# Optimization experiments

Hardware: AMD Instinct MI355X
Metric: run time of the kernel (lower is better)

The kernel has to match this reference:

```python
import jax, jax.numpy as jnp
import numpy as np

B, N, K, H = 512, 8192, 16, 16


def setup_inputs() -> dict:
    key = jax.random.key(0)
    ks = jax.random.split(key, 6)
    x = (2.0 * jax.random.bernoulli(ks[0], 0.5, (B, N)) - 1.0).astype(jnp.float32)
    neighs = jax.random.randint(ks[1], (N, K), 0, N, dtype=jnp.int32)  # per-site neighbor lists
    s1 = 1.0 / np.sqrt(K)
    s2 = 1.0 / np.sqrt(H)
    W1 = jax.random.uniform(ks[2], (N, K, H), jnp.float32, -s1, s1)
    b1 = jax.random.uniform(ks[3], (N, H), jnp.float32, -s1, s1)
    W2 = jax.random.uniform(ks[4], (N, H), jnp.float32, -s2, s2)
    b2 = jax.random.uniform(ks[5], (N,), jnp.float32, -s2, s2)
    return {"x": x, "neighs": neighs, "W1": W1, "b1": b1, "W2": W2, "b2": b2}


def reference(x, neighs, W1, b1, W2, b2):
    # Vectorized form of: for each site n, gather its K neighbors from x,
    # run a site-specific MLP [K -> H -> 1] (ReLU hidden, sigmoid output),
    # and scatter the scalar into x_hat[:, n].
    gathered = x[:, neighs]                                   # [B, N, K]
    h = jax.nn.relu(jnp.einsum('bnk,nkh->bnh', gathered, W1) + b1)  # [B, N, H]
    x_hat = jax.nn.sigmoid(jnp.einsum('bnh,nh->bn', h, W2) + b2)    # [B, N]
    return x_hat
```

## Files before the change

kernel.cpp:

```cpp
#include <hip/hip_runtime.h>
#include <stdint.h>

#define BB 512
#define NN 8192
#define KK 16
#define HH 16

typedef _Float16 f16;
typedef _Float16 f16x4 __attribute__((ext_vector_type(4)));
typedef float f32x4 __attribute__((ext_vector_type(4)));
typedef uint32_t u32x2 __attribute__((ext_vector_type(2)));

__global__ __launch_bounds__(256) void pack_kernel(const float* __restrict__ x,
                                                   uint32_t* __restrict__ xpT) {
    const int j = blockIdx.x * 256 + threadIdx.x;
    const int w = blockIdx.y;
    uint32_t word = 0u;
#pragma unroll
    for (int i = 0; i < 32; ++i)
        word |= (x[(size_t)(w * 32 + i) * NN + j] > 0.0f ? 1u : 0u) << i;
    xpT[(size_t)j * 16 + w] = word;
}

__global__ __launch_bounds__(256, 4) void mfma_kernel(
    const uint32_t* __restrict__ xpT, const int* __restrict__ neighs,
    const float* __restrict__ W1, const float* __restrict__ b1,
    const float* __restrict__ W2, const float* __restrict__ b2,
    float* __restrict__ out) {
    __shared__ int jtab[4][64];
    __shared__ __align__(16) uint32_t wbuf[4][4][32];
    __shared__ float tile[64][20];

    const int tid = threadIdx.x;
    const int wv  = __builtin_amdgcn_readfirstlane(tid >> 6);
    const int l   = tid & 63;
    const int l15 = l & 15;
    const int lg  = l >> 4;
    const int n0  = blockIdx.x * 16;
    const int b0  = blockIdx.y * 64;
    const int w0  = blockIdx.y * 2;

    jtab[wv][l] = neighs[(n0 + wv * 4) * KK + l];

#pragma unroll
    for (int ni = 0; ni < 4; ++ni) {
        const int n = n0 + wv * 4 + ni;

        if (l < 32) {
            const int j = jtab[wv][ni * 16 + (l & 15)];
            wbuf[wv][ni][l] = xpT[(size_t)j * 16 + w0 + (l >> 4)];
        }

        const float* W1n = W1 + (size_t)n * (KK * HH) + lg * 4 * HH + l15;
        f16x4 a;
#pragma unroll
        for (int i = 0; i < 4; ++i) a[i] = (f16)W1n[i * HH];

        const float4 b1v = *(const float4*)(b1 + (size_t)n * HH + lg * 4);
        const f32x4 cinit = {b1v.x, b1v.y, b1v.z, b1v.w};
        const float4 w2v = *(const float4*)(W2 + (size_t)n * HH + lg * 4);
        const float b2n = b2[n];

#pragma unroll
        for (int tb = 0; tb < 4; ++tb) {
            const uint4 wk =
                *(const uint4*)&wbuf[wv][ni][(tb >> 1) * 16 + lg * 4];
            const int pos = (tb & 1) * 16 + l15;
            const uint32_t d0 = 0xBC00BC00u ^ (((wk.x >> pos) & 1u) << 15) ^
                                (((wk.y >> pos) & 1u) << 31);
            const uint32_t d1 = 0xBC00BC00u ^ (((wk.z >> pos) & 1u) << 15) ^
                                (((wk.w >> pos) & 1u) << 31);
            const u32x2 bd = {d0, d1};
            const f16x4 bfr = __builtin_bit_cast(f16x4, bd);

            const f32x4 acc =
                __builtin_amdgcn_mfma_f32_16x16x16f16(a, bfr, cinit, 0, 0, 0);

            float z = fmaf(fmaxf(acc[0], 0.f), w2v.x,
                      fmaf(fmaxf(acc[1], 0.f), w2v.y,
                      fmaf(fmaxf(acc[2], 0.f), w2v.z,
                           fmaxf(acc[3], 0.f) * w2v.w)));
            z += __shfl_xor(z, 16);
            z += __shfl_xor(z, 32);
            z += b2n;
            const float r = 1.0f / (1.0f + __expf(-z));
            if (l < 16) tile[tb * 16 + l][wv * 4 + ni] = r;
        }
    }
    __syncthreads();

    const int row = tid >> 2;
    const int cg  = tid & 3;
    const float4 v = *(const float4*)&tile[row][cg * 4];
    *(float4*)(out + (size_t)(b0 + row) * NN + n0 + cg * 4) = v;
}

__global__ __launch_bounds__(512) void scalar_kernel(
    const float* __restrict__ x, const int* __restrict__ neighs,
    const float* __restrict__ W1, const float* __restrict__ b1,
    const float* __restrict__ W2, const float* __restrict__ b2,
    float* __restrict__ outp) {
    const int n = blockIdx.x;
    const int b = threadIdx.x;
    const int* nb = neighs + n * KK;
    const float* W1n = W1 + (size_t)n * KK * HH;
    const float* b1n = b1 + (size_t)n * HH;
    const float* W2n = W2 + (size_t)n * HH;

    float s[KK];
#pragma unroll
    for (int k = 0; k < KK; ++k) s[k] = x[(size_t)b * NN + nb[k]];

    float acc[HH];
#pragma unroll
    for (int h = 0; h < HH; ++h) acc[h] = b1n[h];
#pragma unroll
    for (int k = 0; k < KK; ++k)
#pragma unroll
        for (int h = 0; h < HH; ++h)
            acc[h] = fmaf(s[k], W1n[k * HH + h], acc[h]);

    float z = b2[n];
#pragma unroll
    for (int h = 0; h < HH; ++h)
        z = fmaf(fmaxf(acc[h], 0.0f), W2n[h], z);
    outp[(size_t)b * NN + n] = 1.0f / (1.0f + __expf(-z));
}

extern "C" void kernel_launch(void* const* d_in, const int* in_sizes, int n_in,
                              void* d_out, int out_size, void* d_ws, size_t ws_size,
                              hipStream_t stream) {
    const float* x      = (const float*)d_in[0];
    const int*   neighs = (const int*)d_in[1];
    const float* W1     = (const float*)d_in[2];
    const float* b1     = (const float*)d_in[3];
    const float* W2     = (const float*)d_in[4];
    const float* b2     = (const float*)d_in[5];
    float* out = (float*)d_out;

    const size_t pack_bytes = (size_t)NN * 16 * sizeof(uint32_t);

    if (ws_size >= pack_bytes) {
        uint32_t* xpT = (uint32_t*)d_ws;
        pack_kernel<<<dim3(NN / 256, BB / 32), 256, 0, stream>>>(x, xpT);
        mfma_kernel<<<dim3(NN / 16, BB / 64), 256, 0, stream>>>(
            xpT, neighs, W1, b1, W2, b2, out);
    } else {
        scalar_kernel<<<NN, BB, 0, stream>>>(x, neighs, W1, b1, W2, b2, out);
    }
}
```

Measured before the change: 31.13 us.

## Process the full batch per block so each site's weights load once

The MFMA kernel grid changes from (N/16, B/64) blocks of 256 threads to N/16 blocks of 512 threads, and each block now covers all 512 batch rows for 16 sites. Each wave handles 2 sites and runs 32 MFMA tiles per site instead of 4. It gathers all 16 packed batch words per neighbour into padded LDS, and the output tile covers 512 rows. This removes the re-reading of W1, b1, W2 and neighbour indices across the 8 batch blocks. In exchange there are fewer, larger blocks, about 40KB more LDS per block, and a long serial MFMA chain per wave.

Result: slower. 34.89 us (+12.1%).

```diff
diff --git a/kernel.cpp b/kernel.cpp
--- a/kernel.cpp
+++ b/kernel.cpp
@@ -22,14 +22,13 @@
     xpT[(size_t)j * 16 + w] = word;
 }
 
-__global__ __launch_bounds__(256, 4) void mfma_kernel(
+__global__ __launch_bounds__(512, 4) void mfma_kernel(
     const uint32_t* __restrict__ xpT, const int* __restrict__ neighs,
     const float* __restrict__ W1, const float* __restrict__ b1,
     const float* __restrict__ W2, const float* __restrict__ b2,
     float* __restrict__ out) {
-    __shared__ int jtab[4][64];
-    __shared__ __align__(16) uint32_t wbuf[4][4][32];
-    __shared__ float tile[64][20];
+    __shared__ __align__(16) uint32_t wbuf[8][2][16 * 20];
+    __shared__ __align__(16) float tile[512][20];
 
     const int tid = threadIdx.x;
     const int wv  = __builtin_amdgcn_readfirstlane(tid >> 6);
@@ -37,18 +36,17 @@
     const int l15 = l & 15;
     const int lg  = l >> 4;
     const int n0  = blockIdx.x * 16;
-    const int b0  = blockIdx.y * 64;
-    const int w0  = blockIdx.y * 2;
-
-    jtab[wv][l] = neighs[(n0 + wv * 4) * KK + l];
 
 #pragma unroll
-    for (int ni = 0; ni < 4; ++ni) {
-        const int n = n0 + wv * 4 + ni;
+    for (int ni = 0; ni < 2; ++ni) {
+        const int n = n0 + wv * 2 + ni;
+        uint32_t* wb = &wbuf[wv][ni][0];
 
-        if (l < 32) {
-            const int j = jtab[wv][ni * 16 + (l & 15)];
-            wbuf[wv][ni][l] = xpT[(size_t)j * 16 + w0 + (l >> 4)];
+#pragma unroll
+        for (int q = 0; q < 4; ++q) {
+            const int k = q * 4 + lg;
+            const int j = neighs[n * KK + k];
+            wb[l15 * 20 + k] = xpT[(size_t)j * 16 + l15];
         }
 
         const float* W1n = W1 + (size_t)n * (KK * HH) + lg * 4 * HH + l15;
@@ -62,10 +60,10 @@
         const float b2n = b2[n];
 
 #pragma unroll
-        for (int tb = 0; tb < 4; ++tb) {
-            const uint4 wk =
-                *(const uint4*)&wbuf[wv][ni][(tb >> 1) * 16 + lg * 4];
+        for (int tb = 0; tb < 32; ++tb) {
+            const int wg  = tb >> 1;
             const int pos = (tb & 1) * 16 + l15;
+            const uint4 wk = *(const uint4*)&wb[wg * 20 + lg * 4];
             const uint32_t d0 = 0xBC00BC00u ^ (((wk.x >> pos) & 1u) << 15) ^
                                 (((wk.y >> pos) & 1u) << 31);
             const uint32_t d1 = 0xBC00BC00u ^ (((wk.z >> pos) & 1u) << 15) ^
@@ -84,15 +82,18 @@
             z += __shfl_xor(z, 32);
             z += b2n;
             const float r = 1.0f / (1.0f + __expf(-z));
-            if (l < 16) tile[tb * 16 + l][wv * 4 + ni] = r;
+            if (l < 16) tile[tb * 16 + l15][wv * 2 + ni] = r;
         }
     }
     __syncthreads();
 
-    const int row = tid >> 2;
-    const int cg  = tid & 3;
-    const float4 v = *(const float4*)&tile[row][cg * 4];
-    *(float4*)(out + (size_t)(b0 + row) * NN + n0 + cg * 4) = v;
+#pragma unroll
+    for (int p = 0; p < 4; ++p) {
+        const int row = (tid >> 2) + p * 128;
+        const int c   = (tid & 3) * 4;
+        const float4 v = *(const float4*)&tile[row][c];
+        *(float4*)(out + (size_t)row * NN + n0 + c) = v;
+    }
 }
 
 __global__ __launch_bounds__(512) void scalar_kernel(
@@ -143,7 +144,7 @@
     if (ws_size >= pack_bytes) {
         uint32_t* xpT = (uint32_t*)d_ws;
         pack_kernel<<<dim3(NN / 256, BB / 32), 256, 0, stream>>>(x, xpT);
-        mfma_kernel<<<dim3(NN / 16, BB / 64), 256, 0, stream>>>(
+        mfma_kernel<<<dim3(NN / 16), 512, 0, stream>>>(
             xpT, neighs, W1, b1, W2, b2, out);
     } else {
         scalar_kernel<<<NN, BB, 0, stream>>>(x, neighs, W1, b1, W2, b2, out);
```
